# Optimization experiments

Measured on AMD Instinct MI355X. Metric: run time of the kernel, lower is better.

Reference implementation:

```python
import jax, jax.numpy as jnp
import numpy as np


def setup_inputs() -> dict:
    key = jax.random.key(0)
    x = jax.random.normal(key, (16, 64, 256, 256), dtype=jnp.float32)
    return {"x": x}


def reference(x):
    # x: [B, C, H, W]
    b, c, h, w = x.shape
    # L2 norm over channel dim -> [B, 1, H, W]
    weights = jnp.sqrt(jnp.sum(x * x, axis=1, keepdims=True))
    # softmax over height (dim=2)
    weights = jax.nn.softmax(weights, axis=2)
    # weighted sum over height -> [B, C, 1, W]
    weighted_sum = jnp.sum(x * weights, axis=2, keepdims=True)
    weight_sum = jnp.sum(weights, axis=2, keepdims=True)  # [B, 1, 1, W]
    compressed = weighted_sum / (weight_sum + 1e-8)
    # broadcast-repeat along height -> [B, C, H, W]
    out = jnp.broadcast_to(compressed, (b, c, h, w))
    return out
```

## Files before the change

kernel.cpp:

```cpp
#include <hip/hip_runtime.h>


constexpr int B = 16, C = 64, H = 256, W = 256;
constexpr int W4 = W / 4;

__global__ __launch_bounds__(256) void k_norm(const float* __restrict__ x,
                                              float* __restrict__ n) {
    int tid = blockIdx.x * 256 + threadIdx.x;
    int w4 = tid & (W4 - 1);
    int h  = (tid >> 6) & (H - 1);
    int b  = tid >> 14;
    const float4* xp = (const float4*)x + (size_t)b * C * H * W4 + (size_t)h * W4 + w4;
    float4 acc = make_float4(0.f, 0.f, 0.f, 0.f);
#pragma unroll 8
    for (int c = 0; c < C; ++c) {
        float4 v = xp[(size_t)c * H * W4];
        acc.x += v.x * v.x; acc.y += v.y * v.y;
        acc.z += v.z * v.z; acc.w += v.w * v.w;
    }
    float4 r = make_float4(sqrtf(acc.x), sqrtf(acc.y), sqrtf(acc.z), sqrtf(acc.w));
    ((float4*)n)[tid] = r;
}

__global__ __launch_bounds__(256) void k_softmax(float* __restrict__ n) {
    __shared__ float tile[H][64];
    __shared__ float red[4][64];
    __shared__ float fin[64];
    int b  = blockIdx.x >> 2;
    int w0 = (blockIdx.x & 3) << 6;
    int t  = threadIdx.x;
    float* base = n + (size_t)b * H * W + w0;

    for (int i = t; i < H * 64; i += 256)
        tile[i >> 6][i & 63] = base[(size_t)(i >> 6) * W + (i & 63)];
    __syncthreads();

    int wl = t & 63, seg = t >> 6;
    float m = -3.4e38f;
    for (int hh = seg * 64; hh < seg * 64 + 64; ++hh)
        m = fmaxf(m, tile[hh][wl]);
    red[seg][wl] = m;
    __syncthreads();
    if (seg == 0)
        fin[wl] = fmaxf(fmaxf(red[0][wl], red[1][wl]), fmaxf(red[2][wl], red[3][wl]));
    __syncthreads();

    float fm = fin[wl];
    float s = 0.f;
    for (int hh = seg * 64; hh < seg * 64 + 64; ++hh) {
        float e = __expf(tile[hh][wl] - fm);
        tile[hh][wl] = e;
        s += e;
    }
    red[seg][wl] = s;
    __syncthreads();
    if (seg == 0) {
        float S = red[0][wl] + red[1][wl] + red[2][wl] + red[3][wl];
        fin[wl] = 1.0f / (S * (1.0f + 1e-8f));
    }
    __syncthreads();

    float iv = fin[wl];
    for (int i = t; i < H * 64; i += 256)
        base[(size_t)(i >> 6) * W + (i & 63)] = tile[i >> 6][i & 63] * iv;
}

__global__ __launch_bounds__(256) void k_wsum(const float* __restrict__ x,
                                              const float* __restrict__ wt,
                                              float* __restrict__ out) {
    __shared__ float4 part[4][64];
    int b = blockIdx.x >> 6;
    int c = blockIdx.x & (C - 1);
    int t = threadIdx.x;
    int w4 = t & 63, hq = t >> 6;

    const float4* xp = (const float4*)x + (size_t)(b * C + c) * H * W4 + w4;
    const float4* wp = (const float4*)wt + (size_t)b * H * W4 + w4;
    float4 acc = make_float4(0.f, 0.f, 0.f, 0.f);
#pragma unroll 8
    for (int hh = hq * 64; hh < hq * 64 + 64; ++hh) {
        float4 xv = xp[(size_t)hh * W4];
        float4 wv = wp[(size_t)hh * W4];
        acc.x += xv.x * wv.x; acc.y += xv.y * wv.y;
        acc.z += xv.z * wv.z; acc.w += xv.w * wv.w;
    }
    part[hq][w4] = acc;
    __syncthreads();
    if (hq == 0) {
        float4 p0 = part[0][w4], p1 = part[1][w4], p2 = part[2][w4], p3 = part[3][w4];
        float4 f;
        f.x = p0.x + p1.x + p2.x + p3.x;
        f.y = p0.y + p1.y + p2.y + p3.y;
        f.z = p0.z + p1.z + p2.z + p3.z;
        f.w = p0.w + p1.w + p2.w + p3.w;
        part[0][w4] = f;
    }
    __syncthreads();
    float4 fin = part[0][w4];
    float4* op = (float4*)out + (size_t)(b * C + c) * H * W4;
    for (int i = t; i < H * W4; i += 256)
        op[i] = fin;
}

extern "C" void kernel_launch(void* const* d_in, const int* in_sizes, int n_in,
                              void* d_out, int out_size, void* d_ws, size_t ws_size,
                              hipStream_t stream) {
    const float* x = (const float*)d_in[0];
    float* out = (float*)d_out;
    float* n = (float*)d_ws;

    k_norm<<<B * H * W4 / 256, 256, 0, stream>>>(x, n);
    k_softmax<<<B * (W / 64), 256, 0, stream>>>(n);
    k_wsum<<<B * C, 256, 0, stream>>>(x, n, out);
}
```

Baseline: 509.8 us.

## Split softmax into stats kernel and fuse exp normalization into weighted sum

Replaces the in-place softmax kernel with a stats kernel that writes only the per-column max and inverse sum. The weighted-sum kernel then recomputes exp(norm - max) on the fly and applies the inverse sum at the end. This removes the shared-tile staging and the write-back of the normalized weights. It adds redundant exp work per channel. The broadcast output writes also become nontemporal stores, to reduce cache pollution.

```diff
diff --git a/kernel.cpp b/kernel.cpp
--- a/kernel.cpp
+++ b/kernel.cpp
@@ -3,6 +3,8 @@
 
 constexpr int B = 16, C = 64, H = 256, W = 256;
 constexpr int W4 = W / 4;
+
+typedef float nfloat4 __attribute__((ext_vector_type(4)));
 
 __global__ __launch_bounds__(256) void k_norm(const float* __restrict__ x,
                                               float* __restrict__ n) {
@@ -22,84 +24,80 @@
     ((float4*)n)[tid] = r;
 }
 
-__global__ __launch_bounds__(256) void k_softmax(float* __restrict__ n) {
-    __shared__ float tile[H][64];
+__global__ __launch_bounds__(256) void k_stats(const float* __restrict__ n,
+                                               float* __restrict__ m,
+                                               float* __restrict__ inv) {
     __shared__ float red[4][64];
-    __shared__ float fin[64];
     int b  = blockIdx.x >> 2;
     int w0 = (blockIdx.x & 3) << 6;
     int t  = threadIdx.x;
-    float* base = n + (size_t)b * H * W + w0;
+    int wl = t & 63, hq = t >> 6;
+    const float* base = n + (size_t)b * H * W + w0 + wl;
 
-    for (int i = t; i < H * 64; i += 256)
-        tile[i >> 6][i & 63] = base[(size_t)(i >> 6) * W + (i & 63)];
+    float mx = -3.4e38f;
+    for (int hh = hq * 64; hh < hq * 64 + 64; ++hh)
+        mx = fmaxf(mx, base[(size_t)hh * W]);
+    red[hq][wl] = mx;
+    __syncthreads();
+    float M = fmaxf(fmaxf(red[0][wl], red[1][wl]), fmaxf(red[2][wl], red[3][wl]));
     __syncthreads();
 
-    int wl = t & 63, seg = t >> 6;
-    float m = -3.4e38f;
-    for (int hh = seg * 64; hh < seg * 64 + 64; ++hh)
-        m = fmaxf(m, tile[hh][wl]);
-    red[seg][wl] = m;
+    float s = 0.f;
+    for (int hh = hq * 64; hh < hq * 64 + 64; ++hh)
+        s += __expf(base[(size_t)hh * W] - M);
+    red[hq][wl] = s;
     __syncthreads();
-    if (seg == 0)
-        fin[wl] = fmaxf(fmaxf(red[0][wl], red[1][wl]), fmaxf(red[2][wl], red[3][wl]));
-    __syncthreads();
-
-    float fm = fin[wl];
-    float s = 0.f;
-    for (int hh = seg * 64; hh < seg * 64 + 64; ++hh) {
-        float e = __expf(tile[hh][wl] - fm);
-        tile[hh][wl] = e;
-        s += e;
+    if (hq == 0) {
+        float S = red[0][wl] + red[1][wl] + red[2][wl] + red[3][wl];
+        m[b * W + w0 + wl]   = M;
+        inv[b * W + w0 + wl] = 1.0f / (S * (1.0f + 1e-8f));
     }
-    red[seg][wl] = s;
-    __syncthreads();
-    if (seg == 0) {
-        float S = red[0][wl] + red[1][wl] + red[2][wl] + red[3][wl];
-        fin[wl] = 1.0f / (S * (1.0f + 1e-8f));
-    }
-    __syncthreads();
-
-    float iv = fin[wl];
-    for (int i = t; i < H * 64; i += 256)
-        base[(size_t)(i >> 6) * W + (i & 63)] = tile[i >> 6][i & 63] * iv;
 }
 
 __global__ __launch_bounds__(256) void k_wsum(const float* __restrict__ x,
-                                              const float* __restrict__ wt,
+                                              const float* __restrict__ n,
+                                              const float* __restrict__ m,
+                                              const float* __restrict__ inv,
                                               float* __restrict__ out) {
-    __shared__ float4 part[4][64];
+    __shared__ float4 red[4][64];
+    __shared__ float4 fin[64];
     int b = blockIdx.x >> 6;
     int c = blockIdx.x & (C - 1);
     int t = threadIdx.x;
     int w4 = t & 63, hq = t >> 6;
 
+    float4 m4   = ((const float4*)(m   + (size_t)b * W))[w4];
+    float4 inv4 = ((const float4*)(inv + (size_t)b * W))[w4];
+    const float4* np = (const float4*)n + (size_t)b * H * W4 + w4;
     const float4* xp = (const float4*)x + (size_t)(b * C + c) * H * W4 + w4;
-    const float4* wp = (const float4*)wt + (size_t)b * H * W4 + w4;
+
     float4 acc = make_float4(0.f, 0.f, 0.f, 0.f);
-#pragma unroll 8
+#pragma unroll 4
     for (int hh = hq * 64; hh < hq * 64 + 64; ++hh) {
         float4 xv = xp[(size_t)hh * W4];
-        float4 wv = wp[(size_t)hh * W4];
-        acc.x += xv.x * wv.x; acc.y += xv.y * wv.y;
-        acc.z += xv.z * wv.z; acc.w += xv.w * wv.w;
+        float4 nv = np[(size_t)hh * W4];
+        acc.x += xv.x * __expf(nv.x - m4.x);
+        acc.y += xv.y * __expf(nv.y - m4.y);
+        acc.z += xv.z * __expf(nv.z - m4.z);
+        acc.w += xv.w * __expf(nv.w - m4.w);
     }
-    part[hq][w4] = acc;
+    red[hq][w4] = acc;
     __syncthreads();
     if (hq == 0) {
-        float4 p0 = part[0][w4], p1 = part[1][w4], p2 = part[2][w4], p3 = part[3][w4];
+        float4 p0 = red[0][w4], p1 = red[1][w4], p2 = red[2][w4], p3 = red[3][w4];
         float4 f;
-        f.x = p0.x + p1.x + p2.x + p3.x;
-        f.y = p0.y + p1.y + p2.y + p3.y;
-        f.z = p0.z + p1.z + p2.z + p3.z;
-        f.w = p0.w + p1.w + p2.w + p3.w;
-        part[0][w4] = f;
+        f.x = (p0.x + p1.x + p2.x + p3.x) * inv4.x;
+        f.y = (p0.y + p1.y + p2.y + p3.y) * inv4.y;
+        f.z = (p0.z + p1.z + p2.z + p3.z) * inv4.z;
+        f.w = (p0.w + p1.w + p2.w + p3.w) * inv4.w;
+        fin[w4] = f;
     }
     __syncthreads();
-    float4 fin = part[0][w4];
-    float4* op = (float4*)out + (size_t)(b * C + c) * H * W4;
+    float4 fv = fin[t & 63];
+    nfloat4 f = { fv.x, fv.y, fv.z, fv.w };
+    nfloat4* op = (nfloat4*)out + (size_t)(b * C + c) * H * W4;
     for (int i = t; i < H * W4; i += 256)
-        op[i] = fin;
+        __builtin_nontemporal_store(f, op + i);
 }
 
 extern "C" void kernel_launch(void* const* d_in, const int* in_sizes, int n_in,
@@ -107,9 +105,11 @@
                               hipStream_t stream) {
     const float* x = (const float*)d_in[0];
     float* out = (float*)d_out;
-    float* n = (float*)d_ws;
+    float* n   = (float*)d_ws;
+    float* m   = n + (size_t)B * H * W;
+    float* inv = m + (size_t)B * W;
 
-    k_norm<<<B * H * W4 / 256, 256, 0, stream>>>(x, n);
-    k_softmax<<<B * (W / 64), 256, 0, stream>>>(n);
-    k_wsum<<<B * C, 256, 0, stream>>>(x, n, out);
+    k_norm <<<B * H * W4 / 256, 256, 0, stream>>>(x, n);
+    k_stats<<<B * (W / 64),     256, 0, stream>>>(n, m, inv);
+    k_wsum <<<B * C,            256, 0, stream>>>(x, n, m, inv, out);
 }
```

Result: no change. 506.9 us (-0.6%).
